# Kernel optimization log

Measured on AMD Instinct MI355X. Metric: run time of the kernel, lower is better.

Reference implementation:

```python
import jax, jax.numpy as jnp
import numpy as np

LEAKY_SLOPE = 0.2
ALPHA, BETA = 1.0, 0.1
CLAMP_MAX = 40.0

N_NODES, N_FEAT = 20000, 128
N_EDGES, N_QUERY = 320000, 200000
B = 512            # boundary matrix size
DIM = 8            # 'dimension' hyperparam


def setup_inputs() -> dict:
    key = jax.random.key(0)
    ks = jax.random.split(key, 20)
    sc = 1.0 / np.sqrt(B)
    inp = {
        'x': jax.random.normal(ks[0], (N_NODES, N_FEAT), jnp.float32),
        'L0': jax.random.normal(ks[1], (B, B), jnp.float32) * sc,
        'L1': jax.random.normal(ks[2], (B, B), jnp.float32) * sc,
        'edge_index': jax.random.randint(ks[3], (2, N_EDGES), 0, N_NODES),
        'total_edges': jax.random.randint(ks[4], (N_QUERY, 2), 0, N_NODES),
        # learned params (Linear weights stored as [in, out])
        'conv1_W': jax.random.normal(ks[5], (N_FEAT, 64), jnp.float32) * 0.05,
        'conv1_b': jnp.zeros((64,), jnp.float32),
        'conv2_W': jax.random.normal(ks[6], (64, 32), jnp.float32) * 0.05,
        'conv2_b': jnp.zeros((32,), jnp.float32),
        'weights_sim': jax.random.normal(ks[7], (2 * B, DIM), jnp.float32) * 0.05,
        'embeddings_sim': jax.random.normal(ks[8], (N_FEAT, 2 * B), jnp.float32) * 0.05,
        'weights_off_diagonal': jax.random.normal(ks[9], (B, B), jnp.float32) * sc,
        'weights_L_0': jax.random.normal(ks[10], (B, 32), jnp.float32) * 0.05,
        'weights_L_1': jax.random.normal(ks[11], (B, 32), jnp.float32) * 0.05,
        'lin1_W': jax.random.normal(ks[12], (DIM + 32, 32), jnp.float32) * 0.1,
        'lin1_b': jnp.zeros((32,), jnp.float32),
        'lin_W': jax.random.normal(ks[13], (32, 1), jnp.float32) * 0.1,
        'lin_b': jnp.zeros((1,), jnp.float32),
    }
    return inp


def _renorm_rows(v):
    # torch renorm_(2, 0, 1): rescale rows whose L2 norm exceeds 1
    n = jnp.linalg.norm(v, axis=1, keepdims=True)
    return v * jnp.where(n > 1.0, 1.0 / (n + 1e-7), 1.0)


def _gcn_conv(h, src, dst, dinv, W, b):
    h = h @ W
    msg = h[src] * (dinv[src] * dinv[dst])[:, None]
    return jax.ops.segment_sum(msg, dst, num_segments=h.shape[0]) + b


def reference(x, L0, L1, edge_index, total_edges,
              conv1_W, conv1_b, conv2_W, conv2_b,
              weights_sim, embeddings_sim, weights_off_diagonal,
              weights_L_0, weights_L_1, lin1_W, lin1_b, lin_W, lin_b):
    N = x.shape[0]
    # --- g_encode: two GCN layers (eval mode, dropout = identity) ---
    loops = jnp.arange(N)
    src = jnp.concatenate([edge_index[0], loops])
    dst = jnp.concatenate([edge_index[1], loops])
    deg = jax.ops.segment_sum(jnp.ones_like(dst, dtype=x.dtype), dst, num_segments=N)
    dinv = jnp.where(deg > 0, jax.lax.rsqrt(jnp.maximum(deg, 1.0)), 0.0)
    h = jax.nn.relu(_gcn_conv(x, src, dst, dinv, conv1_W, conv1_b))
    g_emb = jax.nn.relu(_gcn_conv(h, src, dst, dinv, conv2_W, conv2_b))  # [N, 32]

    # --- s_encode: boundary-matrix block + softmax ---
    L0_r = L0 @ L0
    L1_r = L1 @ L1
    rel = (L0_r @ weights_L_0) @ (L1_r @ weights_L_1).T          # [B, B]
    rel_ = weights_off_diagonal @ rel                             # [B, B]
    upper = jnp.concatenate([L0_r, rel_], axis=1)
    lower = jnp.concatenate([rel_.T, L1_r], axis=1)
    sim_block = jax.nn.softmax(jax.nn.relu(jnp.concatenate([upper, lower], axis=0)), axis=1)  # [2B, 2B]

    s_emb = ((x @ embeddings_sim) @ sim_block) @ weights_sim      # [N, DIM]
    s_emb = _renorm_rows(s_emb)
    g = _renorm_rows(g_emb)

    # --- edge gather + distance MLP ---
    i0, i1 = total_edges[:, 0], total_edges[:, 1]
    d_sim = jnp.square(s_emb[i0] - s_emb[i1])                     # [Eq, DIM]
    g_sq = jnp.square(g[i0] - g[i1])                              # [Eq, 32]
    feat = jnp.concatenate([ALPHA * g_sq, BETA * d_sim], axis=1)  # [Eq, 40]
    hq = jax.nn.leaky_relu(feat @ lin1_W + lin1_b, LEAKY_SLOPE)
    sqdist = jnp.abs(hq @ lin_W + lin_b).reshape(-1)
    sqdist = jnp.clip(sqdist, 0.0, CLAMP_MAX)
    prob = jax.nn.sigmoid(2.0 - sqdist)  # == 1/(exp(sqdist-2)+1)
    return prob
```

## Files before the change

### kernel.cpp

```cpp
#include <hip/hip_runtime.h>
#include <math.h>

#define NE 320000
#define NN 20000
#define NQ 200000

struct Prm {
  const float *x, *L0, *L1;
  const int *ei, *te;
  const float *W1, *b1, *W2, *b2, *wsim, *embs, *wod, *wL0, *wL1, *lin1W, *lin1b, *linW, *linb;
  float *out;
  int *ideg, *start, *cursor, *csr;
  float *dinv, *h1raw, *h2raw, *g, *L0r, *L1r, *U, *V0, *V1, *Ab2, *Bb, *Mm, *Ee, *semb;
};

__device__ __forceinline__ void gemm512_ab(char* smem, const float* __restrict__ A,
                                           const float* __restrict__ B,
                                           float* __restrict__ C, int bb) {
  float (*As)[68] = (float(*)[68])smem;
  float (*Bs)[68] = (float(*)[68])(smem + 16 * 68 * 4);
  int tid = threadIdx.x;
  int tx = tid & 15, ty = tid >> 4;
  int brow = (bb >> 3) * 64;
  int bcol = (bb & 7) * 64;
  float c[4][4] = {};
  for (int k0 = 0; k0 < 512; k0 += 16) {
#pragma unroll
    for (int t = 0; t < 4; t++) {
      int idx = tid * 4 + t;
      int r = idx >> 4, cc = idx & 15;
      As[cc][r] = A[(size_t)(brow + r) * 512 + k0 + cc];
      int r2 = idx >> 6, c2 = idx & 63;
      Bs[r2][c2] = B[(size_t)(k0 + r2) * 512 + bcol + c2];
    }
    __syncthreads();
#pragma unroll
    for (int k = 0; k < 16; k++) {
      float a0 = As[k][ty * 4 + 0], a1 = As[k][ty * 4 + 1];
      float a2 = As[k][ty * 4 + 2], a3 = As[k][ty * 4 + 3];
      float b0 = Bs[k][tx * 4 + 0], b1 = Bs[k][tx * 4 + 1];
      float b2 = Bs[k][tx * 4 + 2], b3 = Bs[k][tx * 4 + 3];
      c[0][0] = fmaf(a0, b0, c[0][0]); c[0][1] = fmaf(a0, b1, c[0][1]);
      c[0][2] = fmaf(a0, b2, c[0][2]); c[0][3] = fmaf(a0, b3, c[0][3]);
      c[1][0] = fmaf(a1, b0, c[1][0]); c[1][1] = fmaf(a1, b1, c[1][1]);
      c[1][2] = fmaf(a1, b2, c[1][2]); c[1][3] = fmaf(a1, b3, c[1][3]);
      c[2][0] = fmaf(a2, b0, c[2][0]); c[2][1] = fmaf(a2, b1, c[2][1]);
      c[2][2] = fmaf(a2, b2, c[2][2]); c[2][3] = fmaf(a2, b3, c[2][3]);
      c[3][0] = fmaf(a3, b0, c[3][0]); c[3][1] = fmaf(a3, b1, c[3][1]);
      c[3][2] = fmaf(a3, b2, c[3][2]); c[3][3] = fmaf(a3, b3, c[3][3]);
    }
    __syncthreads();
  }
#pragma unroll
  for (int i = 0; i < 4; i++)
#pragma unroll
    for (int j = 0; j < 4; j++)
      C[(size_t)(brow + ty * 4 + i) * 512 + bcol + tx * 4 + j] = c[i][j];
}

template<int K, int N>
__device__ __forceinline__ void xw_body(char* smem, const float* __restrict__ X,
                                        const float* __restrict__ W,
                                        float* __restrict__ Y, int bb) {
  constexpr int TPR = N / 4;
  constexpr int ROWS = 256 / TPR;
  float* Wl = (float*)smem;
  for (int t = threadIdx.x; t < K * N / 4; t += 256)
    ((float4*)Wl)[t] = ((const float4*)W)[t];
  __syncthreads();
  int r = bb * ROWS + threadIdx.x / TPR;
  int c4 = (threadIdx.x % TPR) * 4;
  if (r >= NN) return;
  const float4* xr4 = (const float4*)(X + (size_t)r * K);
  float a0 = 0, a1 = 0, a2 = 0, a3 = 0;
#pragma unroll 4
  for (int k4 = 0; k4 < K / 4; k4++) {
    float4 xv = xr4[k4];
    int kb = k4 * 4;
    { const float4 w = *(const float4*)&Wl[(kb + 0) * N + c4];
      a0 = fmaf(xv.x, w.x, a0); a1 = fmaf(xv.x, w.y, a1); a2 = fmaf(xv.x, w.z, a2); a3 = fmaf(xv.x, w.w, a3); }
    { const float4 w = *(const float4*)&Wl[(kb + 1) * N + c4];
      a0 = fmaf(xv.y, w.x, a0); a1 = fmaf(xv.y, w.y, a1); a2 = fmaf(xv.y, w.z, a2); a3 = fmaf(xv.y, w.w, a3); }
    { const float4 w = *(const float4*)&Wl[(kb + 2) * N + c4];
      a0 = fmaf(xv.z, w.x, a0); a1 = fmaf(xv.z, w.y, a1); a2 = fmaf(xv.z, w.z, a2); a3 = fmaf(xv.z, w.w, a3); }
    { const float4 w = *(const float4*)&Wl[(kb + 3) * N + c4];
      a0 = fmaf(xv.w, w.x, a0); a1 = fmaf(xv.w, w.y, a1); a2 = fmaf(xv.w, w.z, a2); a3 = fmaf(xv.w, w.w, a3); }
  }
  float4 o; o.x = a0; o.y = a1; o.z = a2; o.w = a3;
  *(float4*)&Y[(size_t)r * N + c4] = o;
}

__device__ __forceinline__ void sk512_body(const float* X, const float* W, float* Y, int b) {
  int r = b * 32 + threadIdx.x / 8;
  int c4 = (threadIdx.x % 8) * 4;
  const float4* xr4 = (const float4*)(X + (size_t)r * 512);
  float a0 = 0, a1 = 0, a2 = 0, a3 = 0;
#pragma unroll 2
  for (int k4 = 0; k4 < 128; k4++) {
    float4 xv = xr4[k4];
    int kb = k4 * 4;
    { const float4 w = *(const float4*)&W[(kb + 0) * 32 + c4];
      a0 = fmaf(xv.x, w.x, a0); a1 = fmaf(xv.x, w.y, a1); a2 = fmaf(xv.x, w.z, a2); a3 = fmaf(xv.x, w.w, a3); }
    { const float4 w = *(const float4*)&W[(kb + 1) * 32 + c4];
      a0 = fmaf(xv.y, w.x, a0); a1 = fmaf(xv.y, w.y, a1); a2 = fmaf(xv.y, w.z, a2); a3 = fmaf(xv.y, w.w, a3); }
    { const float4 w = *(const float4*)&W[(kb + 2) * 32 + c4];
      a0 = fmaf(xv.z, w.x, a0); a1 = fmaf(xv.z, w.y, a1); a2 = fmaf(xv.z, w.z, a2); a3 = fmaf(xv.z, w.w, a3); }
    { const float4 w = *(const float4*)&W[(kb + 3) * 32 + c4];
      a0 = fmaf(xv.w, w.x, a0); a1 = fmaf(xv.w, w.y, a1); a2 = fmaf(xv.w, w.z, a2); a3 = fmaf(xv.w, w.w, a3); }
  }
  float4 o; o.x = a0; o.y = a1; o.z = a2; o.w = a3;
  *(float4*)&Y[(size_t)r * 32 + c4] = o;
}


__global__ __launch_bounds__(256) void k1(Prm p) {
  __shared__ __align__(16) char smem[32768];
  int b = blockIdx.x;
  if (b < 64)        gemm512_ab(smem, p.L0, p.L0, p.L0r, b);
  else if (b < 128)  gemm512_ab(smem, p.L1, p.L1, p.L1r, b - 64);
  else if (b < 192)  gemm512_ab(smem, p.wod, p.L0, p.U, b - 128);
  else if (b < 208)  sk512_body(p.L0, p.wL0, p.V0, b - 192);
  else if (b < 224)  sk512_body(p.L1, p.wL1, p.V1, b - 208);
  else if (b < 1474) xw_body<128, 64>(smem, p.x, p.W1, p.h1raw, b - 224);
  else {
    int e = (b - 1474) * 256 + threadIdx.x;
    if (e < NE) atomicAdd(&p.ideg[p.ei[NE + e]], 1);
  }
}

__global__ __launch_bounds__(256) void k2(Prm p) {
  int b = blockIdx.x;
  if (b < 16) { sk512_body(p.U, p.V0, p.Ab2, b); return; }
  if (b < 32) { sk512_body(p.L1, p.V1, p.Bb, b - 16); return; }
  __shared__ int wsum[4];
  int tid = threadIdx.x;
  int base = tid * 80;
  int4 c[20];
  int s = 0;
  if (base < NN) {
    const int4* ip = (const int4*)p.ideg + tid * 20;
#pragma unroll
    for (int i = 0; i < 20; i++) c[i] = ip[i];
#pragma unroll
    for (int i = 0; i < 20; i++) s += c[i].x + c[i].y + c[i].z + c[i].w;
  }
  int lane = tid & 63, wid = tid >> 6;
  int v = s;
#pragma unroll
  for (int o = 1; o < 64; o <<= 1) { int u = __shfl_up(v, o); if (lane >= o) v += u; }
  if (lane == 63) wsum[wid] = v;
  __syncthreads();
  int wbase = 0;
  for (int w = 0; w < wid; w++) wbase += wsum[w];
  int off = wbase + v - s;
  if (base < NN) {
#pragma unroll
    for (int i = 0; i < 20; i++) {
      int4 cc = c[i];
      int4 st;
      st.x = off; off += cc.x;
      st.y = off; off += cc.y;
      st.z = off; off += cc.z;
      st.w = off; off += cc.w;
      ((int4*)p.start)[tid * 20 + i] = st;
      ((int4*)p.cursor)[tid * 20 + i] = st;
      float4 dv;
      dv.x = rsqrtf((float)(cc.x + 1));
      dv.y = rsqrtf((float)(cc.y + 1));
      dv.z = rsqrtf((float)(cc.z + 1));
      dv.w = rsqrtf((float)(cc.w + 1));
      ((float4*)p.dinv)[tid * 20 + i] = dv;
    }
  }
}

__global__ __launch_bounds__(256) void k3(Prm p) {
  int b = blockIdx.x;
  int tid = threadIdx.x;
  if (b >= 1024) {
    int e = (b - 1024) * 256 + tid;
    if (e < NE) {
      int d = p.ei[NE + e];
      int pos = atomicAdd(&p.cursor[d], 1);
      p.csr[pos] = p.ei[e];
    }
    return;
  }
  int i = b;
  __shared__ float smax[4];
  __shared__ float sred[4][9];
  float urow[32];
  {
    const float4* up = (const float4*)((i < 512) ? (p.Ab2 + i * 32) : (p.Bb + (i - 512) * 32));
#pragma unroll
    for (int q = 0; q < 8; q++) {
      float4 u4 = up[q];
      urow[q * 4 + 0] = u4.x; urow[q * 4 + 1] = u4.y;
      urow[q * 4 + 2] = u4.z; urow[q * 4 + 3] = u4.w;
    }
  }
  float loc[4];
  float mymax = 0.0f;
#pragma unroll
  for (int tt = 0; tt < 4; tt++) {
    int j = tid + tt * 256;
    float v;
    if (i < 512) {
      if (j < 512) v = p.L0r[i * 512 + j];
      else {
        const float4* bj = (const float4*)(p.Bb + (j - 512) * 32);
        float acc = 0.0f;
#pragma unroll
        for (int q = 0; q < 8; q++) {
          float4 b4 = bj[q];
          acc = fmaf(urow[q * 4 + 0], b4.x, acc); acc = fmaf(urow[q * 4 + 1], b4.y, acc);
          acc = fmaf(urow[q * 4 + 2], b4.z, acc); acc = fmaf(urow[q * 4 + 3], b4.w, acc);
        }
        v = acc;
      }
    } else {
      int r = i - 512;
      if (j < 512) {
        const float4* aj = (const float4*)(p.Ab2 + j * 32);
        float acc = 0.0f;
#pragma unroll
        for (int q = 0; q < 8; q++) {
          float4 a4 = aj[q];
          acc = fmaf(urow[q * 4 + 0], a4.x, acc); acc = fmaf(urow[q * 4 + 1], a4.y, acc);
          acc = fmaf(urow[q * 4 + 2], a4.z, acc); acc = fmaf(urow[q * 4 + 3], a4.w, acc);
        }
        v = acc;
      } else v = p.L1r[r * 512 + (j - 512)];
    }
    v = fmaxf(v, 0.0f);
    loc[tt] = v;
    mymax = fmaxf(mymax, v);
  }
#pragma unroll
  for (int o = 32; o > 0; o >>= 1) mymax = fmaxf(mymax, __shfl_down(mymax, o));
  int wid = tid >> 6, lane = tid & 63;
  if (lane == 0) smax[wid] = mymax;
  __syncthreads();
  float m = fmaxf(fmaxf(smax[0], smax[1]), fmaxf(smax[2], smax[3]));

  float z = 0.0f, pm[8] = {};
#pragma unroll
  for (int tt = 0; tt < 4; tt++) {
    int j = tid + tt * 256;
    float e = __expf(loc[tt] - m);
    z += e;
    const float* wr = p.wsim + j * 8;
#pragma unroll
    for (int d = 0; d < 8; d++) pm[d] = fmaf(e, wr[d], pm[d]);
  }
#pragma unroll
  for (int o = 32; o > 0; o >>= 1) {
    z += __shfl_down(z, o);
#pragma unroll
    for (int d = 0; d < 8; d++) pm[d] += __shfl_down(pm[d], o);
  }
  if (lane == 0) {
    sred[wid][0] = z;
#pragma unroll
    for (int d = 0; d < 8; d++) sred[wid][1 + d] = pm[d];
  }
  __syncthreads();
  if (tid < 8) {
    float zt = sred[0][0] + sred[1][0] + sred[2][0] + sred[3][0];
    float pt = sred[0][1 + tid] + sred[1][1 + tid] + sred[2][1 + tid] + sred[3][1 + tid];
    p.Mm[i * 8 + tid] = pt / zt;
  }
}

__global__ __launch_bounds__(256) void k4(Prm p) {
  __shared__ float W2l[64 * 32];
  __shared__ float h1l[4][64];
  int b = blockIdx.x;
  int tid = threadIdx.x;
  if (b < 5000) {
    for (int u = tid; u < 512; u += 256)
      ((float4*)W2l)[u] = ((const float4*)p.W2)[u];
    __syncthreads();
    int w = tid >> 6;
    int lane = tid & 63;
    int slot = lane >> 4;
    int fi = lane & 15;
    int n = b * 4 + w;
    int s0 = p.start[n], cnt = p.ideg[n];
    float4 acc = {0.f, 0.f, 0.f, 0.f};
    for (int k = 0; k < cnt; k += 4) {
      int kk = k + slot;
      bool valid = kk < cnt;
      int src = valid ? p.csr[s0 + kk] : n;
      float wgt = valid ? p.dinv[src] : 0.0f;
      float4 v = ((const float4*)(p.h1raw + (size_t)src * 64))[fi];
      acc.x = fmaf(v.x, wgt, acc.x); acc.y = fmaf(v.y, wgt, acc.y);
      acc.z = fmaf(v.z, wgt, acc.z); acc.w = fmaf(v.w, wgt, acc.w);
    }
    acc.x += __shfl_xor(acc.x, 16); acc.y += __shfl_xor(acc.y, 16);
    acc.z += __shfl_xor(acc.z, 16); acc.w += __shfl_xor(acc.w, 16);
    acc.x += __shfl_xor(acc.x, 32); acc.y += __shfl_xor(acc.y, 32);
    acc.z += __shfl_xor(acc.z, 32); acc.w += __shfl_xor(acc.w, 32);
    float dn = p.dinv[n];
    float4 self = ((const float4*)(p.h1raw + (size_t)n * 64))[fi];
    float4 b1q = ((const float4*)p.b1)[fi];
    float4 h;
    h.x = fmaxf(fmaf(acc.x, dn, self.x * dn * dn) + b1q.x, 0.0f);
    h.y = fmaxf(fmaf(acc.y, dn, self.y * dn * dn) + b1q.y, 0.0f);
    h.z = fmaxf(fmaf(acc.z, dn, self.z * dn * dn) + b1q.z, 0.0f);
    h.w = fmaxf(fmaf(acc.w, dn, self.w * dn * dn) + b1q.w, 0.0f);
    if (slot == 0) ((float4*)h1l[w])[fi] = h;
    __syncthreads();
    int c = lane & 31, half = lane >> 5;
    float s = 0.0f;
    const float* hr = h1l[w];
#pragma unroll
    for (int kk2 = 0; kk2 < 32; kk2++) {
      int k = half * 32 + kk2;
      s = fmaf(hr[k], W2l[k * 32 + c], s);
    }
    s += __shfl_xor(s, 32);
    if (half == 0) p.h2raw[(size_t)n * 32 + c] = s;
    return;
  }
  int lane = tid & 63;
  int r = (b - 5000) * 4 + (tid >> 6);
  const float* er = p.embs + (size_t)r * 1024;
  float acc[8] = {};
  for (int it = 0; it < 16; it++) {
    int k = lane + it * 64;
    float e = er[k];
    const float4* mp = (const float4*)&p.Mm[k * 8];
    float4 m0 = mp[0], m1 = mp[1];
    acc[0] = fmaf(e, m0.x, acc[0]); acc[1] = fmaf(e, m0.y, acc[1]);
    acc[2] = fmaf(e, m0.z, acc[2]); acc[3] = fmaf(e, m0.w, acc[3]);
    acc[4] = fmaf(e, m1.x, acc[4]); acc[5] = fmaf(e, m1.y, acc[5]);
    acc[6] = fmaf(e, m1.z, acc[6]); acc[7] = fmaf(e, m1.w, acc[7]);
  }
#pragma unroll
  for (int o = 32; o > 0; o >>= 1)
#pragma unroll
    for (int d = 0; d < 8; d++) acc[d] += __shfl_down(acc[d], o);
  if (lane == 0)
#pragma unroll
    for (int d = 0; d < 8; d++) p.Ee[r * 8 + d] = acc[d];
}

__global__ __launch_bounds__(256) void k5(Prm p) {
  __shared__ float El[1024];
  int b = blockIdx.x;
  int tid = threadIdx.x;
  if (b < 5000) {
    int w = tid >> 6;
    int lane = tid & 63;
    int slot = lane >> 3;
    int fi = lane & 7;
    int n = b * 4 + w;
    int s0 = p.start[n], cnt = p.ideg[n];
    float4 acc = {0.f, 0.f, 0.f, 0.f};
    for (int k = 0; k < cnt; k += 8) {
      int kk = k + slot;
      bool valid = kk < cnt;
      int src = valid ? p.csr[s0 + kk] : n;
      float wgt = valid ? p.dinv[src] : 0.0f;
      float4 v = ((const float4*)(p.h2raw + (size_t)src * 32))[fi];
      acc.x = fmaf(v.x, wgt, acc.x); acc.y = fmaf(v.y, wgt, acc.y);
      acc.z = fmaf(v.z, wgt, acc.z); acc.w = fmaf(v.w, wgt, acc.w);
    }
    acc.x += __shfl_xor(acc.x, 8);  acc.y += __shfl_xor(acc.y, 8);
    acc.z += __shfl_xor(acc.z, 8);  acc.w += __shfl_xor(acc.w, 8);
    acc.x += __shfl_xor(acc.x, 16); acc.y += __shfl_xor(acc.y, 16);
    acc.z += __shfl_xor(acc.z, 16); acc.w += __shfl_xor(acc.w, 16);
    acc.x += __shfl_xor(acc.x, 32); acc.y += __shfl_xor(acc.y, 32);
    acc.z += __shfl_xor(acc.z, 32); acc.w += __shfl_xor(acc.w, 32);
    float dn = p.dinv[n];
    float4 self = ((const float4*)(p.h2raw + (size_t)n * 32))[fi];
    float4 b2q = ((const float4*)p.b2)[fi];
    float4 h;
    h.x = fmaxf(fmaf(acc.x, dn, self.x * dn * dn) + b2q.x, 0.0f);
    h.y = fmaxf(fmaf(acc.y, dn, self.y * dn * dn) + b2q.y, 0.0f);
    h.z = fmaxf(fmaf(acc.z, dn, self.z * dn * dn) + b2q.z, 0.0f);
    h.w = fmaxf(fmaf(acc.w, dn, self.w * dn * dn) + b2q.w, 0.0f);
    float n2 = h.x * h.x + h.y * h.y + h.z * h.z + h.w * h.w;
    n2 += __shfl_xor(n2, 1); n2 += __shfl_xor(n2, 2); n2 += __shfl_xor(n2, 4);
    float nrm = sqrtf(n2);
    float sc = (nrm > 1.0f) ? 1.0f / (nrm + 1e-7f) : 1.0f;
    if (slot == 0) {
      float4 o; o.x = h.x * sc; o.y = h.y * sc; o.z = h.z * sc; o.w = h.w * sc;
      ((float4*)(p.g + (size_t)n * 32))[fi] = o;
    }
    return;
  }
  for (int u = tid; u < 256; u += 256)
    ((float4*)El)[u] = ((const float4*)p.Ee)[u];
  __syncthreads();
  int row = (b - 5000) * 256 + tid;
  if (row >= NN) return;
  const float4* xr4 = (const float4*)(p.x + (size_t)row * 128);
  float s[8] = {};
#pragma unroll 4
  for (int k4 = 0; k4 < 32; k4++) {
    float4 xv = xr4[k4];
    int kb = k4 * 4;
#pragma unroll
    for (int u = 0; u < 4; u++) {
      float xk = (u == 0) ? xv.x : (u == 1) ? xv.y : (u == 2) ? xv.z : xv.w;
      const float4* ep = (const float4*)&El[(kb + u) * 8];
      float4 e0 = ep[0], e1 = ep[1];
      s[0] = fmaf(xk, e0.x, s[0]); s[1] = fmaf(xk, e0.y, s[1]);
      s[2] = fmaf(xk, e0.z, s[2]); s[3] = fmaf(xk, e0.w, s[3]);
      s[4] = fmaf(xk, e1.x, s[4]); s[5] = fmaf(xk, e1.y, s[5]);
      s[6] = fmaf(xk, e1.z, s[6]); s[7] = fmaf(xk, e1.w, s[7]);
    }
  }
  float n2 = 0.0f;
#pragma unroll
  for (int d = 0; d < 8; d++) n2 += s[d] * s[d];
  float n = sqrtf(n2);
  float sc = (n > 1.0f) ? 1.0f / (n + 1e-7f) : 1.0f;
#pragma unroll
  for (int d = 0; d < 8; d++) p.semb[(size_t)row * 8 + d] = s[d] * sc;
}

__global__ __launch_bounds__(256) void k6(Prm p) {
  int q = blockIdx.x * 256 + threadIdx.x;
  if (q >= NQ) return;
  const int2 pr = ((const int2*)p.te)[q];
  int i0 = pr.x, i1 = pr.y;
  float feat[40];
  const float4* g0 = (const float4*)(p.g + (size_t)i0 * 32);
  const float4* g1 = (const float4*)(p.g + (size_t)i1 * 32);
#pragma unroll
  for (int u = 0; u < 8; u++) {
    float4 a = g0[u], b = g1[u];
    float d0 = a.x - b.x, d1 = a.y - b.y, d2 = a.z - b.z, d3 = a.w - b.w;
    feat[u * 4 + 0] = d0 * d0; feat[u * 4 + 1] = d1 * d1;
    feat[u * 4 + 2] = d2 * d2; feat[u * 4 + 3] = d3 * d3;
  }
  const float4* s0 = (const float4*)(p.semb + (size_t)i0 * 8);
  const float4* s1 = (const float4*)(p.semb + (size_t)i1 * 8);
#pragma unroll
  for (int u = 0; u < 2; u++) {
    float4 a = s0[u], b = s1[u];
    float d0 = a.x - b.x, d1 = a.y - b.y, d2 = a.z - b.z, d3 = a.w - b.w;
    feat[32 + u * 4 + 0] = 0.1f * d0 * d0; feat[32 + u * 4 + 1] = 0.1f * d1 * d1;
    feat[32 + u * 4 + 2] = 0.1f * d2 * d2; feat[32 + u * 4 + 3] = 0.1f * d3 * d3;
  }
  float acc[32];
#pragma unroll
  for (int c = 0; c < 32; c++) acc[c] = p.lin1b[c];
#pragma unroll
  for (int k = 0; k < 40; k++) {
    float f = feat[k];
#pragma unroll
    for (int c = 0; c < 32; c++) acc[c] = fmaf(f, p.lin1W[k * 32 + c], acc[c]);
  }
  float accv = p.linb[0];
#pragma unroll
  for (int c = 0; c < 32; c++) {
    float a = acc[c];
    a = (a > 0.0f) ? a : 0.2f * a;
    accv = fmaf(a, p.linW[c], accv);
  }
  float sq = fminf(fabsf(accv), 40.0f);
  p.out[q] = 1.0f / (1.0f + __expf(sq - 2.0f));
}

extern "C" void kernel_launch(void* const* d_in, const int* in_sizes, int n_in,
                              void* d_out, int out_size, void* d_ws, size_t ws_size,
                              hipStream_t stream) {
  Prm p;
  p.x     = (const float*)d_in[0];
  p.L0    = (const float*)d_in[1];
  p.L1    = (const float*)d_in[2];
  p.ei    = (const int*)d_in[3];
  p.te    = (const int*)d_in[4];
  p.W1    = (const float*)d_in[5];
  p.b1    = (const float*)d_in[6];
  p.W2    = (const float*)d_in[7];
  p.b2    = (const float*)d_in[8];
  p.wsim  = (const float*)d_in[9];
  p.embs  = (const float*)d_in[10];
  p.wod   = (const float*)d_in[11];
  p.wL0   = (const float*)d_in[12];
  p.wL1   = (const float*)d_in[13];
  p.lin1W = (const float*)d_in[14];
  p.lin1b = (const float*)d_in[15];
  p.linW  = (const float*)d_in[16];
  p.linb  = (const float*)d_in[17];
  p.out   = (float*)d_out;

  p.ideg   = (int*)d_ws;
  p.start  = p.ideg + 20000;
  p.cursor = p.start + 20000;
  p.csr    = p.cursor + 20000;
  p.dinv   = (float*)(p.csr + 320000);
  p.h1raw  = p.dinv + 20000;
  p.h2raw  = p.h1raw + 1280000;
  p.g      = p.h2raw + 640000;
  p.L0r    = p.g + 640000;
  p.L1r    = p.L0r + 262144;
  p.U      = p.L1r + 262144;
  p.V0     = p.U + 262144;
  p.V1     = p.V0 + 16384;
  p.Ab2    = p.V1 + 16384;
  p.Bb     = p.Ab2 + 16384;
  p.Mm     = p.Bb + 16384;
  p.Ee     = p.Mm + 8192;
  p.semb   = p.Ee + 1024;

  hipMemsetAsync(p.ideg, 0, 20000 * sizeof(int), stream);
  k1<<<2724, 256, 0, stream>>>(p);
  k2<<<33,   256, 0, stream>>>(p);
  k3<<<2274, 256, 0, stream>>>(p);
  k4<<<5032, 256, 0, stream>>>(p);
  k5<<<5079, 256, 0, stream>>>(p);
  k6<<<782,  256, 0, stream>>>(p);
}
```

Measured before the change: 157.4 us.

## Reassociate boundary-matrix products and split-K the 512x512 squaring GEMMs

The full 512x512 GEMM wod@L0 is dropped. It is replaced by a chain of thin products, L0@(L0@wL0) followed by wod@S0, which removes one of the three large GEMMs. The L0@L0 and L1@L1 GEMMs are split four ways along K into 512 blocks writing partial buffers. A new pass in k2 sums those partials, which adds memory traffic and an extra kernel stage but spreads the work over many more CUs. The x@W1 projection now reads W1 directly from global/cache instead of staging it in shared memory, and the extra thin product gets its own kernel alongside CSR fill.

```diff
diff --git a/kernel.cpp b/kernel.cpp
--- a/kernel.cpp
+++ b/kernel.cpp
@@ -11,12 +11,12 @@
   const float *W1, *b1, *W2, *b2, *wsim, *embs, *wod, *wL0, *wL1, *lin1W, *lin1b, *linW, *linb;
   float *out;
   int *ideg, *start, *cursor, *csr;
-  float *dinv, *h1raw, *h2raw, *g, *L0r, *L1r, *U, *V0, *V1, *Ab2, *Bb, *Mm, *Ee, *semb;
+  float *dinv, *h1raw, *h2raw, *g, *L0r, *L1r, *T0, *T1, *S0, *Bb, *Ab2, *Mm, *Ee, *semb, *Cpart;
 };
 
-__device__ __forceinline__ void gemm512_ab(char* smem, const float* __restrict__ A,
-                                           const float* __restrict__ B,
-                                           float* __restrict__ C, int bb) {
+__device__ __forceinline__ void gemm512_part(char* smem, const float* __restrict__ A,
+                                             const float* __restrict__ B,
+                                             float* __restrict__ C, int bb, int kbase) {
   float (*As)[68] = (float(*)[68])smem;
   float (*Bs)[68] = (float(*)[68])(smem + 16 * 68 * 4);
   int tid = threadIdx.x;
@@ -24,7 +24,7 @@
   int brow = (bb >> 3) * 64;
   int bcol = (bb & 7) * 64;
   float c[4][4] = {};
-  for (int k0 = 0; k0 < 512; k0 += 16) {
+  for (int k0 = kbase; k0 < kbase + 128; k0 += 16) {
 #pragma unroll
     for (int t = 0; t < 4; t++) {
       int idx = tid * 4 + t;
@@ -59,31 +59,27 @@
 }
 
 template<int K, int N>
-__device__ __forceinline__ void xw_body(char* smem, const float* __restrict__ X,
-                                        const float* __restrict__ W,
-                                        float* __restrict__ Y, int bb) {
+__device__ __forceinline__ void xw_stream(const float* __restrict__ X,
+                                          const float* __restrict__ W,
+                                          float* __restrict__ Y, int bb, int M) {
   constexpr int TPR = N / 4;
   constexpr int ROWS = 256 / TPR;
-  float* Wl = (float*)smem;
-  for (int t = threadIdx.x; t < K * N / 4; t += 256)
-    ((float4*)Wl)[t] = ((const float4*)W)[t];
-  __syncthreads();
   int r = bb * ROWS + threadIdx.x / TPR;
   int c4 = (threadIdx.x % TPR) * 4;
-  if (r >= NN) return;
+  if (r >= M) return;
   const float4* xr4 = (const float4*)(X + (size_t)r * K);
   float a0 = 0, a1 = 0, a2 = 0, a3 = 0;
 #pragma unroll 4
   for (int k4 = 0; k4 < K / 4; k4++) {
     float4 xv = xr4[k4];
     int kb = k4 * 4;
-    { const float4 w = *(const float4*)&Wl[(kb + 0) * N + c4];
+    { const float4 w = *(const float4*)&W[(kb + 0) * N + c4];
       a0 = fmaf(xv.x, w.x, a0); a1 = fmaf(xv.x, w.y, a1); a2 = fmaf(xv.x, w.z, a2); a3 = fmaf(xv.x, w.w, a3); }
-    { const float4 w = *(const float4*)&Wl[(kb + 1) * N + c4];
+    { const float4 w = *(const float4*)&W[(kb + 1) * N + c4];
       a0 = fmaf(xv.y, w.x, a0); a1 = fmaf(xv.y, w.y, a1); a2 = fmaf(xv.y, w.z, a2); a3 = fmaf(xv.y, w.w, a3); }
-    { const float4 w = *(const float4*)&Wl[(kb + 2) * N + c4];
+    { const float4 w = *(const float4*)&W[(kb + 2) * N + c4];
       a0 = fmaf(xv.z, w.x, a0); a1 = fmaf(xv.z, w.y, a1); a2 = fmaf(xv.z, w.z, a2); a3 = fmaf(xv.z, w.w, a3); }
-    { const float4 w = *(const float4*)&Wl[(kb + 3) * N + c4];
+    { const float4 w = *(const float4*)&W[(kb + 3) * N + c4];
       a0 = fmaf(xv.w, w.x, a0); a1 = fmaf(xv.w, w.y, a1); a2 = fmaf(xv.w, w.z, a2); a3 = fmaf(xv.w, w.w, a3); }
   }
   float4 o; o.x = a0; o.y = a1; o.z = a2; o.w = a3;
@@ -114,26 +110,44 @@
 
 
 __global__ __launch_bounds__(256) void k1(Prm p) {
-  __shared__ __align__(16) char smem[32768];
+  __shared__ __align__(16) char smem[8704];
   int b = blockIdx.x;
-  if (b < 64)        gemm512_ab(smem, p.L0, p.L0, p.L0r, b);
-  else if (b < 128)  gemm512_ab(smem, p.L1, p.L1, p.L1r, b - 64);
-  else if (b < 192)  gemm512_ab(smem, p.wod, p.L0, p.U, b - 128);
-  else if (b < 208)  sk512_body(p.L0, p.wL0, p.V0, b - 192);
-  else if (b < 224)  sk512_body(p.L1, p.wL1, p.V1, b - 208);
-  else if (b < 1474) xw_body<128, 64>(smem, p.x, p.W1, p.h1raw, b - 224);
+  if (b < 512) {
+    int slice = b & 3, tile = (b >> 2) & 63, g = b >> 8;
+    const float* A = g ? p.L1 : p.L0;
+    float* C = p.Cpart + (size_t)slice * 524288 + (size_t)g * 262144;
+    gemm512_part(smem, A, A, C, tile, slice * 128);
+  }
+  else if (b < 528)  sk512_body(p.L0, p.wL0, p.T0, b - 512);
+  else if (b < 544)  sk512_body(p.L1, p.wL1, p.T1, b - 528);
+  else if (b < 1794) xw_stream<128, 64>(p.x, p.W1, p.h1raw, b - 544, NN);
   else {
-    int e = (b - 1474) * 256 + threadIdx.x;
+    int e = (b - 1794) * 256 + threadIdx.x;
     if (e < NE) atomicAdd(&p.ideg[p.ei[NE + e]], 1);
   }
 }
 
 __global__ __launch_bounds__(256) void k2(Prm p) {
   int b = blockIdx.x;
-  if (b < 16) { sk512_body(p.U, p.V0, p.Ab2, b); return; }
-  if (b < 32) { sk512_body(p.L1, p.V1, p.Bb, b - 16); return; }
+  int tid = threadIdx.x;
+  if (b < 512) {
+    int i4 = b * 256 + tid;
+    const float4* cp = (const float4*)p.Cpart;
+    float4 a = cp[i4];
+    float4 b1 = cp[131072 + i4];
+    float4 c = cp[262144 + i4];
+    float4 d = cp[393216 + i4];
+    float4 o;
+    o.x = a.x + b1.x + c.x + d.x;
+    o.y = a.y + b1.y + c.y + d.y;
+    o.z = a.z + b1.z + c.z + d.z;
+    o.w = a.w + b1.w + c.w + d.w;
+    ((float4*)p.L0r)[i4] = o;
+    return;
+  }
+  if (b < 528) { sk512_body(p.L0, p.T0, p.S0, b - 512); return; }
+  if (b < 544) { sk512_body(p.L1, p.T1, p.Bb, b - 528); return; }
   __shared__ int wsum[4];
-  int tid = threadIdx.x;
   int base = tid * 80;
   int4 c[20];
   int s = 0;
@@ -176,17 +190,18 @@
 
 __global__ __launch_bounds__(256) void k3(Prm p) {
   int b = blockIdx.x;
+  if (b < 16) { sk512_body(p.wod, p.S0, p.Ab2, b); return; }
+  int e = (b - 16) * 256 + threadIdx.x;
+  if (e < NE) {
+    int d = p.ei[NE + e];
+    int pos = atomicAdd(&p.cursor[d], 1);
+    p.csr[pos] = p.ei[e];
+  }
+}
+
+__global__ __launch_bounds__(256) void k4(Prm p) {
+  int i = blockIdx.x;
   int tid = threadIdx.x;
-  if (b >= 1024) {
-    int e = (b - 1024) * 256 + tid;
-    if (e < NE) {
-      int d = p.ei[NE + e];
-      int pos = atomicAdd(&p.cursor[d], 1);
-      p.csr[pos] = p.ei[e];
-    }
-    return;
-  }
-  int i = b;
   __shared__ float smax[4];
   __shared__ float sred[4][9];
   float urow[32];
@@ -272,7 +287,7 @@
   }
 }
 
-__global__ __launch_bounds__(256) void k4(Prm p) {
+__global__ __launch_bounds__(256) void k5(Prm p) {
   __shared__ float W2l[64 * 32];
   __shared__ float h1l[4][64];
   int b = blockIdx.x;
@@ -346,7 +361,7 @@
     for (int d = 0; d < 8; d++) p.Ee[r * 8 + d] = acc[d];
 }
 
-__global__ __launch_bounds__(256) void k5(Prm p) {
+__global__ __launch_bounds__(256) void k6(Prm p) {
   __shared__ float El[1024];
   int b = blockIdx.x;
   int tid = threadIdx.x;
@@ -422,7 +437,7 @@
   for (int d = 0; d < 8; d++) p.semb[(size_t)row * 8 + d] = s[d] * sc;
 }
 
-__global__ __launch_bounds__(256) void k6(Prm p) {
+__global__ __launch_bounds__(256) void k7(Prm p) {
   int q = blockIdx.x * 256 + threadIdx.x;
   if (q >= NQ) return;
   const int2 pr = ((const int2*)p.te)[q];
@@ -500,20 +515,22 @@
   p.g      = p.h2raw + 640000;
   p.L0r    = p.g + 640000;
   p.L1r    = p.L0r + 262144;
-  p.U      = p.L1r + 262144;
-  p.V0     = p.U + 262144;
-  p.V1     = p.V0 + 16384;
-  p.Ab2    = p.V1 + 16384;
-  p.Bb     = p.Ab2 + 16384;
-  p.Mm     = p.Bb + 16384;
+  p.T0     = p.L1r + 262144;
+  p.T1     = p.T0 + 16384;
+  p.S0     = p.T1 + 16384;
+  p.Bb     = p.S0 + 16384;
+  p.Ab2    = p.Bb + 16384;
+  p.Mm     = p.Ab2 + 16384;
   p.Ee     = p.Mm + 8192;
   p.semb   = p.Ee + 1024;
+  p.Cpart  = p.semb + 160000;
 
   hipMemsetAsync(p.ideg, 0, 20000 * sizeof(int), stream);
-  k1<<<2724, 256, 0, stream>>>(p);
-  k2<<<33,   256, 0, stream>>>(p);
-  k3<<<2274, 256, 0, stream>>>(p);
-  k4<<<5032, 256, 0, stream>>>(p);
-  k5<<<5079, 256, 0, stream>>>(p);
-  k6<<<782,  256, 0, stream>>>(p);
-}
+  k1<<<3044, 256, 0, stream>>>(p);
+  k2<<<545,  256, 0, stream>>>(p);
+  k3<<<1266, 256, 0, stream>>>(p);
+  k4<<<1024, 256, 0, stream>>>(p);
+  k5<<<5032, 256, 0, stream>>>(p);
+  k6<<<5079, 256, 0, stream>>>(p);
+  k7<<<782,  256, 0, stream>>>(p);
+}
```

Measured after the change: 184.5 us. 1.17x slower.
